# Kernel optimization log

Hardware: AMD Instinct MI355X
Metric: run time of the kernel (lower is better)

Reference implementation:

```python
import jax, jax.numpy as jnp
import numpy as np

EMBED_DIM = 768
NUM_HEADS = 12
HEAD_DIM = EMBED_DIM // NUM_HEADS


def setup_inputs() -> dict:
    key = jax.random.key(0)
    ks = jax.random.split(key, 12)
    B, T, D, Hp, Wp = 4, 32, EMBED_DIM, 16, 16
    h = jax.random.normal(ks[0], (B, T, D, Hp, Wp), dtype=jnp.float32)
    u_enc = jax.random.uniform(ks[1], (B, T, D, Hp, Wp), dtype=jnp.float32)
    lam = jax.random.uniform(ks[2], (B, T, 1, Hp, Wp), dtype=jnp.float32)
    s = 1.0 / np.sqrt(D)
    Wq = jax.random.normal(ks[3], (D, D), dtype=jnp.float32) * s
    bq = jnp.zeros((D,), dtype=jnp.float32)
    Wk = jax.random.normal(ks[4], (D, D), dtype=jnp.float32) * s
    bk = jnp.zeros((D,), dtype=jnp.float32)
    Wv = jax.random.normal(ks[5], (D, D), dtype=jnp.float32) * s
    bv = jnp.zeros((D,), dtype=jnp.float32)
    Wo = jax.random.normal(ks[6], (D, D), dtype=jnp.float32) * s
    bo = jnp.zeros((D,), dtype=jnp.float32)
    return {"h": h, "u_enc": u_enc, "lam": lam,
            "Wq": Wq, "bq": bq, "Wk": Wk, "bk": bk,
            "Wv": Wv, "bv": bv, "Wo": Wo, "bo": bo}


def reference(h, u_enc, lam, Wq, bq, Wk, bk, Wv, bv, Wo, bo):
    B, T, D, Hp, Wp = h.shape
    S = Hp * Wp
    NH, HD = NUM_HEADS, HEAD_DIM
    # (B,T,D,Hp,Wp) -> (B*S, T, D)
    h_seq = jnp.transpose(h, (0, 3, 4, 1, 2)).reshape(B * S, T, D)
    u_seq = jnp.transpose(u_enc, (0, 3, 4, 1, 2)).reshape(B * S, T, D)
    lam_seq = jnp.transpose(lam, (0, 3, 4, 1, 2)).reshape(B * S, T)
    # projections (nn.Linear: x @ W.T + b)
    Q = (h_seq @ Wq.T + bq).reshape(B * S, T, NH, HD).transpose(0, 2, 1, 3)
    K = (h_seq @ Wk.T + bk).reshape(B * S, T, NH, HD).transpose(0, 2, 1, 3)
    V = (h_seq @ Wv.T + bv).reshape(B * S, T, NH, HD).transpose(0, 2, 1, 3)
    scores = jnp.einsum('bhqd,bhkd->bhqk', Q, K) / jnp.sqrt(jnp.float32(HD))
    # key-dependent uncertainty penalty: lam_j * mean_d(u_j)
    u_pen = lam_seq * u_seq.mean(axis=-1)  # (B*S, T)
    scores = scores - u_pen[:, None, None, :]
    attn = jax.nn.softmax(scores, axis=-1)  # dropout: eval mode (identity)
    out = jnp.einsum('bhqk,bhkd->bhqd', attn, V)
    out = out.transpose(0, 2, 1, 3).reshape(B * S, T, D)
    out = out @ Wo.T + bo
    return jnp.transpose(out.reshape(B, Hp, Wp, T, D), (0, 3, 4, 1, 2))
```

## Files before the change

kernel.cpp:

```cpp
#include <hip/hip_runtime.h>

typedef float   f32x4 __attribute__((ext_vector_type(4)));
typedef _Float16 f16x8 __attribute__((ext_vector_type(8)));
typedef _Float16 f16x4 __attribute__((ext_vector_type(4)));

#define DEV static __device__ __forceinline__

#define BB 4
#define TT 32
#define DD 768
#define SS 256
#define NHD 12
#define HD 64
#define NSEQ  (BB*SS)
#define MTOK  (NSEQ*TT)

DEV void async_copy16(const _Float16* g, _Float16* l) {
  __builtin_amdgcn_global_load_lds(
      (const __attribute__((address_space(1))) unsigned int*)g,
      (__attribute__((address_space(3))) unsigned int*)l,
      16, 0, 0);
}

DEV int swz_chunk(int r, int kc) {
  return r * 4 + (kc ^ (r & 3) ^ ((r >> 2) & 3));
}

__global__ __launch_bounds__(256) void k_transpose_h(const float* __restrict__ h,
                                                     _Float16* __restrict__ A) {
  __shared__ _Float16 Tl[256 * 65];
  const int slab = blockIdx.x;
  const int d0   = blockIdx.y * 64;
  const int t    = threadIdx.x;
  const float4* hv = (const float4*)(h + (slab * DD + d0) * SS);
  #pragma unroll
  for (int i = 0; i < 16; ++i) {
    int dd = i * 4 + (t >> 6);
    int s4 = (t & 63) * 4;
    float4 v = hv[dd * 64 + (t & 63)];
    Tl[(s4 + 0) * 65 + dd] = (_Float16)v.x;
    Tl[(s4 + 1) * 65 + dd] = (_Float16)v.y;
    Tl[(s4 + 2) * 65 + dd] = (_Float16)v.z;
    Tl[(s4 + 3) * 65 + dd] = (_Float16)v.w;
  }
  __syncthreads();
  #pragma unroll
  for (int p = 0; p < 8; ++p) {
    int s  = p * 32 + (t >> 3);
    int dd = (t & 7) * 8;
    f16x8 val;
    #pragma unroll
    for (int j = 0; j < 8; ++j) val[j] = Tl[s * 65 + dd + j];
    *(f16x8*)(A + (slab * SS + s) * DD + d0 + dd) = val;
  }
}

__global__ __launch_bounds__(256) void k_convert_w(const float* __restrict__ Wq,
                                                   const float* __restrict__ Wk,
                                                   const float* __restrict__ Wv,
                                                   const float* __restrict__ Wo,
                                                   _Float16* __restrict__ WQKV,
                                                   _Float16* __restrict__ WoH) {
  int idx = blockIdx.x * 256 + threadIdx.x;
  int row = idx / 96;
  int c8  = (idx % 96) * 8;
  const float* src; _Float16* dst;
  if (row < 768)       { src = Wq + row * 768;          dst = WQKV + row * 768; }
  else if (row < 1536) { src = Wk + (row - 768) * 768;  dst = WQKV + row * 768; }
  else if (row < 2304) { src = Wv + (row - 1536) * 768; dst = WQKV + row * 768; }
  else                 { src = Wo + (row - 2304) * 768; dst = WoH  + (row - 2304) * 768; }
  float4 v0 = *(const float4*)(src + c8);
  float4 v1 = *(const float4*)(src + c8 + 4);
  f16x8 o;
  o[0]=(_Float16)v0.x; o[1]=(_Float16)v0.y; o[2]=(_Float16)v0.z; o[3]=(_Float16)v0.w;
  o[4]=(_Float16)v1.x; o[5]=(_Float16)v1.y; o[6]=(_Float16)v1.z; o[7]=(_Float16)v1.w;
  *(f16x8*)(dst + c8) = o;
}

__global__ __launch_bounds__(256) void k_upen(const float* __restrict__ u,
                                              const float* __restrict__ lam,
                                              float* __restrict__ upen) {
  int slab = blockIdx.x >> 2;
  int q    = blockIdx.x & 3;
  int s    = threadIdx.x;
  const float* base = u + (slab * DD + q * 192) * SS + s;
  float sum = 0.f;
  for (int d = 0; d < 192; ++d) sum += base[d * SS];
  int b = slab >> 5, tt = slab & 31;
  float l = lam[slab * SS + s];
  atomicAdd(&upen[(b * SS + s) * TT + tt], sum * l * (1.0f / 768.0f));
}

#define KSTEP(IT, VM, DO_STG)                                                  \
  {                                                                            \
    const int bt_ = (IT) & 3;                                                  \
    const _Float16* Ac = &sh.g.As[bt_][0];                                     \
    const _Float16* Bc = &sh.g.Bs[bt_][0];                                     \
    f16x8 af[8], bf[4];                                                        \
    _Pragma("unroll")                                                          \
    for (int mi = 0; mi < 8; ++mi) {                                           \
      int row = wm * 128 + mi * 16 + (lane & 15);                              \
      af[mi] = *(const f16x8*)&Ac[(row * 4 + ((lane >> 4) ^ (row & 3))) * 8];  \
    }                                                                          \
    _Pragma("unroll")                                                          \
    for (int ni = 0; ni < 4; ++ni) {                                           \
      int row = wn * 64 + ni * 16 + (lane & 15);                               \
      bf[ni] = *(const f16x8*)&Bc[(row * 4 + ((lane >> 4) ^ (row & 3))) * 8];  \
    }                                                                          \
    if (DO_STG) {                                                              \
      const int kn_ = ((IT) + 3) * 32;                                         \
      stage(A, m0, &sh.g.As[((IT) + 3) & 3][0], kn_);                          \
      stage(Bw, n0, &sh.g.Bs[((IT) + 3) & 3][0], kn_);                         \
    }                                                                          \
    __builtin_amdgcn_s_barrier();                                              \
    asm volatile("s_waitcnt lgkmcnt(0)" ::: "memory");                         \
    __builtin_amdgcn_sched_barrier(0);                                         \
    __builtin_amdgcn_s_setprio(1);                                             \
    _Pragma("unroll")                                                          \
    for (int mi = 0; mi < 8; ++mi)                                             \
      _Pragma("unroll")                                                        \
      for (int ni = 0; ni < 4; ++ni)                                           \
        acc[mi][ni] = __builtin_amdgcn_mfma_f32_16x16x32_f16(bf[ni], af[mi],   \
                                                             acc[mi][ni], 0, 0, 0); \
    __builtin_amdgcn_s_setprio(0);                                             \
    asm volatile("s_waitcnt " VM ::: "memory");                                \
    __builtin_amdgcn_sched_barrier(0);                                         \
    __builtin_amdgcn_s_barrier();                                              \
  }

__global__ __launch_bounds__(512, 2) void k_gemm_qkv(const _Float16* __restrict__ A,
                                                     const _Float16* __restrict__ Bw,
                                                     const float* __restrict__ bq,
                                                     const float* __restrict__ bk,
                                                     const float* __restrict__ bv,
                                                     _Float16* __restrict__ Qp,
                                                     _Float16* __restrict__ Kp,
                                                     _Float16* __restrict__ Vp) {
  __shared__ __align__(16) union ShMem {
    struct { _Float16 As[4][256 * 32]; _Float16 Bs[4][256 * 32]; } g;
    _Float16 Ct[256 * 264];
  } sh;
  const int swz = (blockIdx.x & 7) * 144 + (blockIdx.x >> 3);
  const int mt = swz / 9, nt = swz - mt * 9;
  const int m0 = mt * 256, n0 = nt * 256;
  const int tid = threadIdx.x, lane = tid & 63, w = tid >> 6;
  const int wm = w >> 2, wn = w & 3;
  f32x4 acc[8][4] = {};

  auto stage = [&](const _Float16* __restrict__ g, int grow0, _Float16* l, int k0) {
    #pragma unroll
    for (int li = 0; li < 2; ++li) {
      int cc = tid + 512 * li;
      int row = cc >> 2;
      int kc = (cc & 3) ^ (row & 3);
      async_copy16(g + (grow0 + row) * DD + k0 + kc * 8, l + cc * 8);
    }
  };

  stage(A, m0, &sh.g.As[0][0], 0);  stage(Bw, n0, &sh.g.Bs[0][0], 0);
  stage(A, m0, &sh.g.As[1][0], 32); stage(Bw, n0, &sh.g.Bs[1][0], 32);
  stage(A, m0, &sh.g.As[2][0], 64); stage(Bw, n0, &sh.g.Bs[2][0], 64);
  asm volatile("s_waitcnt vmcnt(8)" ::: "memory");
  __builtin_amdgcn_sched_barrier(0);
  __builtin_amdgcn_s_barrier();

  for (int it = 0; it < 21; ++it) KSTEP(it, "vmcnt(8)", 1);
  KSTEP(21, "vmcnt(4)", 0);
  KSTEP(22, "vmcnt(0)", 0);
  KSTEP(23, "vmcnt(0)", 0);

  const int sel = nt / 3;
  const float scale = (sel == 0) ? 0.125f : 1.0f;
  const float* bias = (sel == 0) ? bq : ((sel == 1) ? bk : bv);
  _Float16* dst = (sel == 0) ? Qp : ((sel == 1) ? Kp : Vp);
  const int b = mt >> 5, t = mt & 31;
  const int nbias0 = nt * 256 - sel * 768;

  #pragma unroll
  for (int ni = 0; ni < 4; ++ni) {
    int n_l = wn * 64 + ni * 16 + (lane >> 4) * 4;
    float4 bsv = *(const float4*)&bias[nbias0 + n_l];
    #pragma unroll
    for (int mi = 0; mi < 8; ++mi) {
      int s = wm * 128 + mi * 16 + (lane & 15);
      f32x4 v = acc[mi][ni];
      f16x4 pk;
      pk[0] = (_Float16)((v[0] + bsv.x) * scale);
      pk[1] = (_Float16)((v[1] + bsv.y) * scale);
      pk[2] = (_Float16)((v[2] + bsv.z) * scale);
      pk[3] = (_Float16)((v[3] + bsv.w) * scale);
      *(f16x4*)&sh.Ct[s * 264 + n_l] = pk;
    }
  }
  __syncthreads();
  const long sbase = ((long)b * 256) * 24576 + (long)t * 64;
  #pragma unroll
  for (int rep = 0; rep < 16; ++rep) {
    int id = rep * 512 + tid;
    int s = id >> 5, c8 = id & 31;
    int n = c8 * 8;
    f16x8 v = *(const f16x8*)&sh.Ct[s * 264 + n];
    int n768 = nbias0 + n;
    int head = n768 >> 6, hd = n768 & 63;
    *(f16x8*)&dst[sbase + (long)s * 24576 + (long)head * 2048 + hd] = v;
  }
}

__global__ __launch_bounds__(256) void k_attn(const _Float16* __restrict__ Qp,
                                              const _Float16* __restrict__ Kp,
                                              const _Float16* __restrict__ Vp,
                                              const float* __restrict__ upen,
                                              _Float16* __restrict__ O) {
  __shared__ _Float16 lds[4][32 * 66 + 32 * 40];
  const int w = threadIdx.x >> 6, lane = threadIdx.x & 63;
  const int seq = blockIdx.x / 3, hg = blockIdx.x % 3;
  const int head = hg * 4 + w;
  const int b = seq >> 8, s = seq & 255;
  _Float16* Vs = &lds[w][0];
  _Float16* Ps = &lds[w][32 * 66];
  const long base = (long)(seq * NHD + head) * 2048;
  const _Float16* Qb = Qp + base;
  const _Float16* Kb = Kp + base;
  const _Float16* Vb = Vp + base;

  {
    int t = lane & 31, hh = (lane >> 5) * 32;
    f16x8 vc[4];
    #pragma unroll
    for (int c = 0; c < 4; ++c) vc[c] = *(const f16x8*)(Vb + t * 64 + hh + c * 8);
    #pragma unroll
    for (int c = 0; c < 4; ++c)
      #pragma unroll
      for (int p = 0; p < 4; ++p) {
        union { _Float16 h[2]; unsigned u; } pk;
        pk.h[0] = vc[c][2 * p]; pk.h[1] = vc[c][2 * p + 1];
        *(unsigned*)&Vs[t * 66 + hh + c * 8 + 2 * p] = pk.u;
      }
  }
  f16x8 qf[2][2], kf[2][2];
  #pragma unroll
  for (int i = 0; i < 2; ++i)
    #pragma unroll
    for (int ks = 0; ks < 2; ++ks) {
      int off = (i * 16 + (lane & 15)) * 64 + ks * 32 + (lane >> 4) * 8;
      qf[i][ks] = *(const f16x8*)(Qb + off);
      kf[i][ks] = *(const f16x8*)(Kb + off);
    }
  f32x4 sc[2][2] = {};
  #pragma unroll
  for (int mq = 0; mq < 2; ++mq)
    #pragma unroll
    for (int nk = 0; nk < 2; ++nk)
      #pragma unroll
      for (int ks = 0; ks < 2; ++ks)
        sc[mq][nk] = __builtin_amdgcn_mfma_f32_16x16x32_f16(qf[mq][ks], kf[nk][ks], sc[mq][nk], 0, 0, 0);

  const float up0 = upen[seq * TT + (lane & 15)];
  const float up1 = upen[seq * TT + 16 + (lane & 15)];

  #pragma unroll
  for (int mq = 0; mq < 2; ++mq) {
    #pragma unroll
    for (int r = 0; r < 4; ++r) {
      float s0 = sc[mq][0][r] - up0;
      float s1 = sc[mq][1][r] - up1;
      float mx = fmaxf(s0, s1);
      #pragma unroll
      for (int off = 1; off < 16; off <<= 1) mx = fmaxf(mx, __shfl_xor(mx, off, 64));
      float e0 = __expf(s0 - mx), e1 = __expf(s1 - mx);
      float sum = e0 + e1;
      #pragma unroll
      for (int off = 1; off < 16; off <<= 1) sum += __shfl_xor(sum, off, 64);
      float inv = 1.0f / sum;
      int row = mq * 16 + (lane >> 4) * 4 + r;
      Ps[row * 40 + (lane & 15)]      = (_Float16)(e0 * inv);
      Ps[row * 40 + 16 + (lane & 15)] = (_Float16)(e1 * inv);
    }
  }
  f16x8 pf[2];
  #pragma unroll
  for (int mq = 0; mq < 2; ++mq)
    pf[mq] = *(const f16x8*)(Ps + (mq * 16 + (lane & 15)) * 40 + (lane >> 4) * 8);
  f32x4 oacc[2][4] = {};
  #pragma unroll
  for (int nh = 0; nh < 4; ++nh) {
    int hd = nh * 16 + (lane & 15);
    f16x8 vf;
    #pragma unroll
    for (int j = 0; j < 8; ++j) vf[j] = Vs[((lane >> 4) * 8 + j) * 66 + hd];
    #pragma unroll
    for (int mq = 0; mq < 2; ++mq)
      oacc[mq][nh] = __builtin_amdgcn_mfma_f32_16x16x32_f16(pf[mq], vf, oacc[mq][nh], 0, 0, 0);
  }
  #pragma unroll
  for (int mq = 0; mq < 2; ++mq)
    #pragma unroll
    for (int nh = 0; nh < 4; ++nh) {
      int hd = nh * 16 + (lane & 15);
      #pragma unroll
      for (int r = 0; r < 4; ++r) {
        int t = mq * 16 + (lane >> 4) * 4 + r;
        O[((long)((b << 5) + t) * SS + s) * DD + head * HD + hd] = (_Float16)oacc[mq][nh][r];
      }
    }
}

__global__ __launch_bounds__(256, 2) void k_gemm_out(const _Float16* __restrict__ Wn,
                                                     const _Float16* __restrict__ O,
                                                     const float* __restrict__ bo,
                                                     float* __restrict__ out) {
  __shared__ _Float16 As[128 * 32];
  __shared__ _Float16 Bs[256 * 32];
  const int ct = blockIdx.x & 127, rt = blockIdx.x >> 7;
  const int R0 = rt * 128, C0 = ct * 256;
  const int tid = threadIdx.x, w = tid >> 6, lane = tid & 63;
  const int wr = (w >> 1) * 64, wcc = (w & 1) * 128;
  f32x4 acc[4][8] = {};
  for (int it = 0; it < 24; ++it) {
    const int k0 = it * 32;
    __syncthreads();
    #pragma unroll
    for (int i = 0; i < 2; ++i) {
      int c = tid + 256 * i;
      int row = c >> 2;
      int coff = ((c & 3) ^ (row & 3) ^ ((row >> 2) & 3)) * 8;
      _Float16* ldsA = (_Float16*)((char*)As + (w * 1024 + i * 4096 + lane * 16));
      async_copy16(Wn + (R0 + row) * DD + k0 + coff, ldsA);
    }
    #pragma unroll
    for (int i = 0; i < 4; ++i) {
      int c = tid + 256 * i;
      int row = c >> 2;
      int coff = ((c & 3) ^ (row & 3) ^ ((row >> 2) & 3)) * 8;
      _Float16* ldsB = (_Float16*)((char*)Bs + (w * 1024 + i * 4096 + lane * 16));
      async_copy16(O + (C0 + row) * DD + k0 + coff, ldsB);
    }
    __syncthreads();
    f16x8 af[4], bf[8];
    #pragma unroll
    for (int ri = 0; ri < 4; ++ri)
      af[ri] = *(const f16x8*)&As[swz_chunk(wr + ri * 16 + (lane & 15), lane >> 4) * 8];
    #pragma unroll
    for (int ci = 0; ci < 8; ++ci)
      bf[ci] = *(const f16x8*)&Bs[swz_chunk(wcc + ci * 16 + (lane & 15), lane >> 4) * 8];
    #pragma unroll
    for (int ri = 0; ri < 4; ++ri)
      #pragma unroll
      for (int ci = 0; ci < 8; ++ci)
        acc[ri][ci] = __builtin_amdgcn_mfma_f32_16x16x32_f16(af[ri], bf[ci], acc[ri][ci], 0, 0, 0);
  }
  const int slab = ct;
  #pragma unroll
  for (int ri = 0; ri < 4; ++ri) {
    #pragma unroll
    for (int ci = 0; ci < 8; ++ci) {
      int s = wcc + ci * 16 + (lane & 15);
      f32x4 v = acc[ri][ci];
      #pragma unroll
      for (int r = 0; r < 4; ++r) {
        int R = R0 + wr + ri * 16 + (lane >> 4) * 4 + r;
        out[((long)slab * DD + R) * SS + s] = v[r] + bo[R];
      }
    }
  }
}

extern "C" void kernel_launch(void* const* d_in, const int* in_sizes, int n_in,
                              void* d_out, int out_size, void* d_ws, size_t ws_size,
                              hipStream_t stream) {
  const float* h   = (const float*)d_in[0];
  const float* u   = (const float*)d_in[1];
  const float* lam = (const float*)d_in[2];
  const float* Wq  = (const float*)d_in[3];
  const float* bq  = (const float*)d_in[4];
  const float* Wk  = (const float*)d_in[5];
  const float* bk  = (const float*)d_in[6];
  const float* Wv  = (const float*)d_in[7];
  const float* bv  = (const float*)d_in[8];
  const float* Wo  = (const float*)d_in[9];
  const float* bo  = (const float*)d_in[10];
  float* out = (float*)d_out;

  char* ws = (char*)d_ws;
  _Float16* Abuf = (_Float16*)(ws);
  _Float16* WQKV = (_Float16*)(ws + 50331648);
  _Float16* WoH  = (_Float16*)(ws + 53870592);
  float*    upen = (float*)   (ws + 55050240);
  _Float16* Qp   = (_Float16*)(ws + 55181312);
  _Float16* Kp   = (_Float16*)(ws + 105512960);
  _Float16* Vp   = (_Float16*)(ws + 155844608);

  hipMemsetAsync(upen, 0, 32768 * sizeof(float), stream);
  k_transpose_h<<<dim3(128, 12), 256, 0, stream>>>(h, Abuf);
  k_convert_w<<<1152, 256, 0, stream>>>(Wq, Wk, Wv, Wo, WQKV, WoH);
  k_upen<<<512, 256, 0, stream>>>(u, lam, upen);
  k_gemm_qkv<<<1152, 512, 0, stream>>>(Abuf, WQKV, bq, bk, bv, Qp, Kp, Vp);
  k_attn<<<1024 * 3, 256, 0, stream>>>(Qp, Kp, Vp, upen, Abuf);
  k_gemm_out<<<128 * 6, 256, 0, stream>>>(WoH, Abuf, bo, out);
}
```

Before: 524.5 us.

## Restructure QKV GEMM loop to one barrier per k-step and refine LDS swizzle

The QKV GEMM main loop now waits on the global-to-LDS copy and hits a single barrier at the top of each k-step. It then issues the prefetch into the buffer freed by the previous step, before reading fragments and running the MFMAs. This drops the second barrier, the explicit lgkmcnt wait, the sched_barriers and the setprio calls, so staging can overlap with compute more freely. It also adds an extra XOR term `((row>>2)&1)` to the LDS chunk swizzle, in both the stage and the read paths, to cut bank conflicts on fragment loads. A __syncthreads is added before the epilogue reuses shared memory. The risk is that losing the explicit scheduling hints lets the compiler interleave instructions less favourably.

```diff
diff --git a/kernel.cpp b/kernel.cpp
--- a/kernel.cpp
+++ b/kernel.cpp
@@ -91,8 +91,15 @@
   atomicAdd(&upen[(b * SS + s) * TT + tt], sum * l * (1.0f / 768.0f));
 }
 
-#define KSTEP(IT, VM, DO_STG)                                                  \
+#define QSTEP(IT, VM, DO_STG)                                                  \
   {                                                                            \
+    asm volatile("s_waitcnt " VM ::: "memory");                                \
+    asm volatile("s_barrier" ::: "memory");                                    \
+    if (DO_STG) {                                                              \
+      const int kn_ = ((IT) + 3) * 32;                                         \
+      stage(A, m0, &sh.g.As[((IT) + 3) & 3][0], kn_);                          \
+      stage(Bw, n0, &sh.g.Bs[((IT) + 3) & 3][0], kn_);                         \
+    }                                                                          \
     const int bt_ = (IT) & 3;                                                  \
     const _Float16* Ac = &sh.g.As[bt_][0];                                     \
     const _Float16* Bc = &sh.g.Bs[bt_][0];                                     \
@@ -100,32 +107,21 @@
     _Pragma("unroll")                                                          \
     for (int mi = 0; mi < 8; ++mi) {                                           \
       int row = wm * 128 + mi * 16 + (lane & 15);                              \
-      af[mi] = *(const f16x8*)&Ac[(row * 4 + ((lane >> 4) ^ (row & 3))) * 8];  \
+      int kc = (lane >> 4) ^ (row & 3) ^ ((row >> 2) & 1);                     \
+      af[mi] = *(const f16x8*)&Ac[(row * 4 + kc) * 8];                         \
     }                                                                          \
     _Pragma("unroll")                                                          \
     for (int ni = 0; ni < 4; ++ni) {                                           \
       int row = wn * 64 + ni * 16 + (lane & 15);                               \
-      bf[ni] = *(const f16x8*)&Bc[(row * 4 + ((lane >> 4) ^ (row & 3))) * 8];  \
+      int kc = (lane >> 4) ^ (row & 3) ^ ((row >> 2) & 1);                     \
+      bf[ni] = *(const f16x8*)&Bc[(row * 4 + kc) * 8];                         \
     }                                                                          \
-    if (DO_STG) {                                                              \
-      const int kn_ = ((IT) + 3) * 32;                                         \
-      stage(A, m0, &sh.g.As[((IT) + 3) & 3][0], kn_);                          \
-      stage(Bw, n0, &sh.g.Bs[((IT) + 3) & 3][0], kn_);                         \
-    }                                                                          \
-    __builtin_amdgcn_s_barrier();                                              \
-    asm volatile("s_waitcnt lgkmcnt(0)" ::: "memory");                         \
-    __builtin_amdgcn_sched_barrier(0);                                         \
-    __builtin_amdgcn_s_setprio(1);                                             \
     _Pragma("unroll")                                                          \
     for (int mi = 0; mi < 8; ++mi)                                             \
       _Pragma("unroll")                                                        \
       for (int ni = 0; ni < 4; ++ni)                                           \
         acc[mi][ni] = __builtin_amdgcn_mfma_f32_16x16x32_f16(bf[ni], af[mi],   \
                                                              acc[mi][ni], 0, 0, 0); \
-    __builtin_amdgcn_s_setprio(0);                                             \
-    asm volatile("s_waitcnt " VM ::: "memory");                                \
-    __builtin_amdgcn_sched_barrier(0);                                         \
-    __builtin_amdgcn_s_barrier();                                              \
   }
 
 __global__ __launch_bounds__(512, 2) void k_gemm_qkv(const _Float16* __restrict__ A,
@@ -152,7 +148,7 @@
     for (int li = 0; li < 2; ++li) {
       int cc = tid + 512 * li;
       int row = cc >> 2;
-      int kc = (cc & 3) ^ (row & 3);
+      int kc = (cc & 3) ^ (row & 3) ^ ((row >> 2) & 1);
       async_copy16(g + (grow0 + row) * DD + k0 + kc * 8, l + cc * 8);
     }
   };
@@ -160,14 +156,11 @@
   stage(A, m0, &sh.g.As[0][0], 0);  stage(Bw, n0, &sh.g.Bs[0][0], 0);
   stage(A, m0, &sh.g.As[1][0], 32); stage(Bw, n0, &sh.g.Bs[1][0], 32);
   stage(A, m0, &sh.g.As[2][0], 64); stage(Bw, n0, &sh.g.Bs[2][0], 64);
-  asm volatile("s_waitcnt vmcnt(8)" ::: "memory");
-  __builtin_amdgcn_sched_barrier(0);
-  __builtin_amdgcn_s_barrier();
-
-  for (int it = 0; it < 21; ++it) KSTEP(it, "vmcnt(8)", 1);
-  KSTEP(21, "vmcnt(4)", 0);
-  KSTEP(22, "vmcnt(0)", 0);
-  KSTEP(23, "vmcnt(0)", 0);
+
+  for (int it = 0; it < 21; ++it) QSTEP(it, "vmcnt(8)", 1);
+  QSTEP(21, "vmcnt(8)", 0);
+  QSTEP(22, "vmcnt(4)", 0);
+  QSTEP(23, "vmcnt(0)", 0);
 
   const int sel = nt / 3;
   const float scale = (sel == 0) ? 0.125f : 1.0f;
@@ -176,6 +169,7 @@
   const int b = mt >> 5, t = mt & 31;
   const int nbias0 = nt * 256 - sel * 768;
 
+  __syncthreads();
   #pragma unroll
   for (int ni = 0; ni < 4; ++ni) {
     int n_l = wn * 64 + ni * 16 + (lane >> 4) * 4;
```

Result: no change. 519.0 us (-1.0%).
